# Performance work log

Hardware: AMD Instinct MI355X
Metric: run time of the kernel (lower is better)

The kernel has to match this reference:

```python
import jax, jax.numpy as jnp
import numpy as np

N_NODES = 50000
N_EDGES = 800000
IN_DIM = 128
HID_DIM = 64
N_HEADS = 4
OUT_DIM = 128
NEG_SLOPE = 0.2  # DGL GATConv default


def gat_conv(x, src, dst, W, attn_l, attn_r, bias, n_nodes):
    """DGL GATConv forward. x:[N,Fin], W:[Fin,H*D], attn_*:[H,D], bias:[H,D]. Returns [N,H,D]."""
    H, D = attn_l.shape
    h = (x @ W).reshape(n_nodes, H, D)              # [N,H,D]
    el = jnp.sum(h * attn_l[None], axis=-1)          # [N,H]
    er = jnp.sum(h * attn_r[None], axis=-1)          # [N,H]
    e = jax.nn.leaky_relu(el[src] + er[dst], NEG_SLOPE)  # [E,H]
    # edge softmax over incoming edges of each dst node (stable)
    m = jax.ops.segment_max(e, dst, num_segments=n_nodes)   # [N,H], -inf for empty
    ex = jnp.exp(e - m[dst])                                 # [E,H]
    denom = jax.ops.segment_sum(ex, dst, num_segments=n_nodes)  # [N,H]
    alpha = ex / denom[dst]                                  # [E,H]
    out = jax.ops.segment_sum(alpha[:, :, None] * h[src], dst, num_segments=n_nodes)
    return out + bias[None]                                  # [N,H,D]


def setup_inputs() -> dict:
    key = jax.random.key(0)
    ks = jax.random.split(key, 12)
    x = jax.random.normal(ks[0], (N_NODES, IN_DIM), dtype=jnp.float32)
    src = jax.random.randint(ks[1], (N_EDGES,), 0, N_NODES, dtype=jnp.int32)
    dst = jax.random.randint(ks[2], (N_EDGES,), 0, N_NODES, dtype=jnp.int32)
    s1 = 1.0 / np.sqrt(IN_DIM)
    s2 = 1.0 / np.sqrt(HID_DIM * N_HEADS)
    W1 = jax.random.normal(ks[3], (IN_DIM, N_HEADS * HID_DIM), dtype=jnp.float32) * s1
    al1 = jax.random.normal(ks[4], (N_HEADS, HID_DIM), dtype=jnp.float32) * 0.1
    ar1 = jax.random.normal(ks[5], (N_HEADS, HID_DIM), dtype=jnp.float32) * 0.1
    b1 = jnp.zeros((N_HEADS, HID_DIM), dtype=jnp.float32)
    W2 = jax.random.normal(ks[6], (N_HEADS * HID_DIM, OUT_DIM), dtype=jnp.float32) * s2
    al2 = jax.random.normal(ks[7], (1, OUT_DIM), dtype=jnp.float32) * 0.1
    ar2 = jax.random.normal(ks[8], (1, OUT_DIM), dtype=jnp.float32) * 0.1
    b2 = jnp.zeros((1, OUT_DIM), dtype=jnp.float32)
    return {"x": x, "src": src, "dst": dst, "W1": W1, "al1": al1, "ar1": ar1,
            "b1": b1, "W2": W2, "al2": al2, "ar2": ar2, "b2": b2}


def reference(x, src, dst, W1, al1, ar1, b1, W2, al2, ar2, b2):
    n = x.shape[0]
    h1 = gat_conv(x, src, dst, W1, al1, ar1, b1, n)          # [N,H,D]
    h1 = jax.nn.relu(h1).reshape(n, -1)                       # [N,H*D]
    h2 = gat_conv(h1, src, dst, W2, al2, ar2, b2, n)          # [N,1,OUT]
    return h2.reshape(n, -1)                                   # [N,OUT]
```

## Files before the change

kernel.cpp:

```cpp
#include <hip/hip_runtime.h>
#include <hip/hip_bf16.h>
#include <math.h>


#define NEG_SLOPE 0.2f
#define NB 256
#define CH 8192

typedef short short8 __attribute__((ext_vector_type(8)));
typedef float float4v __attribute__((ext_vector_type(4)));
typedef float float2v __attribute__((ext_vector_type(2)));

static __device__ __forceinline__ float lrelu(float v) {
    return v > 0.f ? v : NEG_SLOPE * v;
}

static __device__ __forceinline__ unsigned short f2bf(float f) {
    unsigned int u = __float_as_uint(f);
    u = (u + 0x7fffu + ((u >> 16) & 1u)) >> 16;
    return (unsigned short)u;
}
static __device__ __forceinline__ float bf2f(unsigned int lo16) {
    return __uint_as_float(lo16 << 16);
}

static __device__ __forceinline__ int bucket_of(int d, unsigned int M) {
    return (int)(((unsigned long long)(unsigned int)d * M) >> 32);
}

static __device__ __forceinline__ void pk_step(float2v& a00, float2v& a01,
                                               float2v& a10, float2v& a11,
                                               float2v& d0, float2v& d1,
                                               float4 w, unsigned int v) {
    float2v w01; w01[0] = w.x; w01[1] = w.y;
    float2v w23; w23[0] = w.z; w23[1] = w.w;
    float x0 = __uint_as_float(v << 16);
    float x1 = __uint_as_float(v & 0xffff0000u);
    float2v xx0 = {x0, x0};
    float2v xx1 = {x1, x1};
    asm("v_pk_fma_f32 %0, %1, %2, %0" : "+v"(a00) : "v"(w01), "v"(xx0));
    asm("v_pk_fma_f32 %0, %1, %2, %0" : "+v"(a01) : "v"(w23), "v"(xx0));
    asm("v_pk_fma_f32 %0, %1, %2, %0" : "+v"(a10) : "v"(w01), "v"(xx1));
    asm("v_pk_fma_f32 %0, %1, %2, %0" : "+v"(a11) : "v"(w23), "v"(xx1));
    asm("v_pk_add_f32 %0, %1, %0" : "+v"(d0) : "v"(w01));
    asm("v_pk_add_f32 %0, %1, %0" : "+v"(d1) : "v"(w23));
}


__global__ __launch_bounds__(256) void histbin_kernel(
        const int* __restrict__ dst, int* __restrict__ bcnt,
        int E, unsigned int M, int nblk,
        const float* __restrict__ W1, const float* __restrict__ al1,
        const float* __restrict__ ar1, const float* __restrict__ W2,
        const float* __restrict__ al2, const float* __restrict__ ar2,
        unsigned short* __restrict__ W1th, unsigned short* __restrict__ Qt1,
        unsigned short* __restrict__ Qt2, unsigned short* __restrict__ W2t) {
    int b = blockIdx.x;
    int tid = threadIdx.x;
    if (b < nblk) {
        __shared__ int lcnt[NB];
        lcnt[tid] = 0;
        __syncthreads();
        int e0 = b * CH;
        for (int i = tid; i < CH; i += 256) {
            int e = e0 + i;
            if (e < E) atomicAdd(&lcnt[bucket_of(dst[e], M)], 1);
        }
        __syncthreads();
        bcnt[b * NB + tid] = lcnt[tid];
        return;
    }
    int idx = (b - nblk) * 256 + tid;
    if (idx < 32768) {
        int h = idx >> 13;
        int r = idx & 8191;
        int d = r >> 7, k = r & 127;
        W1th[idx] = f2bf(W1[k * 256 + h * 64 + d]);
    } else if (idx < 34816) {
        int j = idx - 32768;
        int c = j >> 7, k = j & 127;
        float s = 0.f;
        if (c < 8) {
            int h = c & 3;
            const float* av = ((c < 4) ? al1 : ar1) + h * 64;
            const float* wrow = W1 + k * 256 + h * 64;
            #pragma unroll 8
            for (int d = 0; d < 64; ++d) s += wrow[d] * av[d];
        }
        Qt1[j] = f2bf(s);
    } else if (idx < 36864) {
        int j = idx - 34816;
        int c = j >> 7, k = j & 127;
        float s = (c == 0) ? al2[k] : (c == 1) ? ar2[k] : 0.f;
        Qt2[j] = f2bf(s);
    } else if (idx < 69632) {
        int j = idx - 36864;
        int m = j >> 8, k = j & 255;
        W2t[(size_t)m * 256 + k] = f2bf(W2[(size_t)k * 128 + m]);
    }
}


__global__ __launch_bounds__(256) void binscan_kernel(
        const int* __restrict__ bcnt, int* __restrict__ cur0,
        int* __restrict__ bucketStart, int nblk, int E) {
    __shared__ int s[NB];
    int t = threadIdx.x;
    int tot = 0;
    for (int blk = 0; blk < nblk; ++blk) tot += bcnt[blk * NB + t];
    s[t] = tot;
    __syncthreads();
    for (int off = 1; off < NB; off <<= 1) {
        int add = (t >= off) ? s[t - off] : 0;
        __syncthreads();
        s[t] += add;
        __syncthreads();
    }
    const int bs = s[t] - tot;
    bucketStart[t] = bs;
    if (t == NB - 1) bucketStart[NB] = E;
    int run = bs;
    for (int blk = 0; blk < nblk; ++blk) {
        int c = bcnt[blk * NB + t];
        cur0[blk * NB + t] = run;
        run += c;
    }
}


__global__ __launch_bounds__(256) void scatxdots_kernel(
        const int* __restrict__ src, const int* __restrict__ dst,
        const int* __restrict__ cur0,
        uint2* __restrict__ pairs, int E, unsigned int M, int nblk,
        const float* __restrict__ x, const unsigned short* __restrict__ Qt,
        unsigned short* __restrict__ xb,
        float* __restrict__ el, float* __restrict__ er, int N) {
    constexpr int KP = 136;
    __shared__ alignas(16) unsigned char smem[(64 + 16) * KP * 2];
    const int tid = threadIdx.x;
    if (blockIdx.x < (unsigned)nblk) {
        int* cur = (int*)smem;
        const int b = blockIdx.x;
        cur[tid] = cur0[b * NB + tid];
        __syncthreads();
        int e0 = b * CH;
        for (int i = tid; i < CH; i += 256) {
            int e = e0 + i;
            if (e < E) {
                int d = dst[e];
                int bk = bucket_of(d, M);
                int pos = atomicAdd(&cur[bk], 1);
                pairs[pos] = make_uint2((unsigned int)src[e], (unsigned int)d);
            }
        }
        return;
    }
    unsigned short* As = (unsigned short*)smem;
    unsigned short* Bs = As + 64 * KP;
    const int wid = tid >> 6, lane = tid & 63;
    const int r0 = (blockIdx.x - nblk) * 64;
    for (int ch = tid; ch < 64 * 16; ch += 256) {
        int row = ch >> 4, kc = ch & 15;
        int gr = r0 + row;
        short8 v = {};
        if (gr < N) {
            float4 a = *(const float4*)(x + (size_t)gr * 128 + kc * 8);
            float4 b = *(const float4*)(x + (size_t)gr * 128 + kc * 8 + 4);
            v[0] = (short)f2bf(a.x); v[1] = (short)f2bf(a.y);
            v[2] = (short)f2bf(a.z); v[3] = (short)f2bf(a.w);
            v[4] = (short)f2bf(b.x); v[5] = (short)f2bf(b.y);
            v[6] = (short)f2bf(b.z); v[7] = (short)f2bf(b.w);
            *(short8*)(xb + (size_t)gr * 128 + kc * 8) = v;
        }
        *(short8*)(As + row * KP + kc * 8) = v;
    }
    {
        int row = tid >> 4, kc = tid & 15;
        *(short8*)(Bs + row * KP + kc * 8) = *(const short8*)(Qt + row * 128 + kc * 8);
    }
    __syncthreads();
    float4v acc = (float4v){0.f, 0.f, 0.f, 0.f};
    const int lr = lane & 15, lk = (lane >> 4) * 8;
    #pragma unroll
    for (int ks = 0; ks < 128; ks += 32) {
        short8 af = *(const short8*)(As + (wid * 16 + lr) * KP + ks + lk);
        short8 bf_ = *(const short8*)(Bs + lr * KP + ks + lk);
        acc = __builtin_amdgcn_mfma_f32_16x16x32_bf16(af, bf_, acc, 0, 0, 0);
    }
    const int rbase = r0 + wid * 16 + (lane >> 4) * 4;
    #pragma unroll
    for (int j = 0; j < 4; ++j) {
        int row = rbase + j;
        if (row < N) {
            if (lr < 4) el[(size_t)row * 4 + lr] = acc[j];
            else if (lr < 8) er[(size_t)row * 4 + (lr - 4)] = acc[j];
        }
    }
}


__global__ __launch_bounds__(256) void bucketcsr_kernel(
        const uint2* __restrict__ pairs, const int* __restrict__ bucketStart,
        int* __restrict__ row_start, int* __restrict__ srcs,
        int N, int npb, int E) {
    __shared__ int cnt[NB];
    __shared__ int sc[NB];
    int b = blockIdx.x;
    int tid = threadIdx.x;
    int nb0 = b * npb;
    int es = bucketStart[b], ee = bucketStart[b + 1];
    cnt[tid] = 0;
    __syncthreads();
    for (int i = es + tid; i < ee; i += 256) {
        uint2 p = pairs[i];
        atomicAdd(&cnt[(int)p.y - nb0], 1);
    }
    __syncthreads();
    int myc = cnt[tid];
    sc[tid] = myc;
    __syncthreads();
    for (int off = 1; off < NB; off <<= 1) {
        int add = (tid >= off) ? sc[tid - off] : 0;
        __syncthreads();
        sc[tid] += add;
        __syncthreads();
    }
    int excl = sc[tid] - myc;
    int n = nb0 + tid;
    if (n < N && tid < npb) row_start[n] = es + excl;
    if (b == gridDim.x - 1 && tid == 0) row_start[N] = E;
    cnt[tid] = es + excl;
    __syncthreads();
    for (int i = es + tid; i < ee; i += 256) {
        uint2 p = pairs[i];
        int pos = atomicAdd(&cnt[(int)p.y - nb0], 1);
        srcs[pos] = (int)p.x;
    }
}


__global__ __launch_bounds__(256) void dots2_kernel(
        const unsigned short* __restrict__ hb, const unsigned short* __restrict__ Qt,
        float* __restrict__ el, float* __restrict__ er, int N) {
    constexpr int KP = 136;
    __shared__ unsigned short As[64 * KP];
    __shared__ unsigned short Bs[16 * KP];
    const int tid = threadIdx.x;
    const int wid = tid >> 6, lane = tid & 63;
    const int r0 = blockIdx.x * 64;
    for (int ch = tid; ch < 64 * 16; ch += 256) {
        int row = ch >> 4, kc = ch & 15;
        int gr = r0 + row;
        short8 v = {};
        if (gr < N) v = *(const short8*)(hb + (size_t)gr * 128 + kc * 8);
        *(short8*)(As + row * KP + kc * 8) = v;
    }
    {
        int row = tid >> 4, kc = tid & 15;
        *(short8*)(Bs + row * KP + kc * 8) = *(const short8*)(Qt + row * 128 + kc * 8);
    }
    __syncthreads();
    float4v acc = (float4v){0.f, 0.f, 0.f, 0.f};
    const int lr = lane & 15, lk = (lane >> 4) * 8;
    #pragma unroll
    for (int ks = 0; ks < 128; ks += 32) {
        short8 af = *(const short8*)(As + (wid * 16 + lr) * KP + ks + lk);
        short8 bf_ = *(const short8*)(Bs + lr * KP + ks + lk);
        acc = __builtin_amdgcn_mfma_f32_16x16x32_bf16(af, bf_, acc, 0, 0, 0);
    }
    const int rbase = r0 + wid * 16 + (lane >> 4) * 4;
    #pragma unroll
    for (int j = 0; j < 4; ++j) {
        int row = rbase + j;
        if (row < N) {
            if (lr == 0) el[row] = acc[j];
            else if (lr == 1) er[row] = acc[j];
        }
    }
}


__global__ __launch_bounds__(256) void agg1x_kernel(const unsigned short* __restrict__ xb,
                            const float* __restrict__ el, const float* __restrict__ er,
                            const int* __restrict__ srcs, const int* __restrict__ row_start,
                            unsigned short* __restrict__ A1, int N) {
    __shared__ int   s_tbl[4][64];
    __shared__ float a_tbl[4][64][4];
    const int wslot = threadIdx.x >> 6;
    const int lane = threadIdx.x & 63;
    const int n = (blockIdx.x * 256 + threadIdx.x) >> 6;
    if (n >= N) return;
    const int rs = row_start[n];
    const int re = row_start[n + 1];

    float2v accP[2][2];
    accP[0][0] = (float2v){0.f, 0.f}; accP[0][1] = (float2v){0.f, 0.f};
    accP[1][0] = (float2v){0.f, 0.f}; accP[1][1] = (float2v){0.f, 0.f};
    float2v dP[2];
    dP[0] = (float2v){0.f, 0.f}; dP[1] = (float2v){0.f, 0.f};

    if (re > rs) {
        const float4 ern = *(const float4*)(er + (size_t)n * 4);
        for (int base = rs; base < re; base += 64) {
            const int cnt = (re - base) < 64 ? (re - base) : 64;
            asm volatile("s_waitcnt lgkmcnt(0)" ::: "memory");
            if (lane < cnt) {
                int sv = srcs[base + lane];
                float4 ev = *(const float4*)(el + (size_t)sv * 4);
                float4 av;
                av.x = __expf(lrelu(ev.x + ern.x));
                av.y = __expf(lrelu(ev.y + ern.y));
                av.z = __expf(lrelu(ev.z + ern.z));
                av.w = __expf(lrelu(ev.w + ern.w));
                s_tbl[wslot][lane] = sv;
                *(float4*)&a_tbl[wslot][lane][0] = av;
            }
            asm volatile("s_waitcnt lgkmcnt(0)" ::: "memory");
            int i = 0;
            for (; i + 4 <= cnt; i += 4) {
                int s0 = s_tbl[wslot][i],     s1 = s_tbl[wslot][i + 1];
                int s2 = s_tbl[wslot][i + 2], s3 = s_tbl[wslot][i + 3];
                float4 w0 = *(const float4*)&a_tbl[wslot][i][0];
                float4 w1 = *(const float4*)&a_tbl[wslot][i + 1][0];
                float4 w2 = *(const float4*)&a_tbl[wslot][i + 2][0];
                float4 w3 = *(const float4*)&a_tbl[wslot][i + 3][0];
                unsigned int v0 = *(const unsigned int*)(xb + (size_t)s0 * 128 + lane * 2);
                unsigned int v1 = *(const unsigned int*)(xb + (size_t)s1 * 128 + lane * 2);
                unsigned int v2 = *(const unsigned int*)(xb + (size_t)s2 * 128 + lane * 2);
                unsigned int v3 = *(const unsigned int*)(xb + (size_t)s3 * 128 + lane * 2);
                pk_step(accP[0][0], accP[0][1], accP[1][0], accP[1][1], dP[0], dP[1], w0, v0);
                pk_step(accP[0][0], accP[0][1], accP[1][0], accP[1][1], dP[0], dP[1], w1, v1);
                pk_step(accP[0][0], accP[0][1], accP[1][0], accP[1][1], dP[0], dP[1], w2, v2);
                pk_step(accP[0][0], accP[0][1], accP[1][0], accP[1][1], dP[0], dP[1], w3, v3);
            }
            for (; i < cnt; ++i) {
                int s0 = s_tbl[wslot][i];
                float4 w = *(const float4*)&a_tbl[wslot][i][0];
                unsigned int v = *(const unsigned int*)(xb + (size_t)s0 * 128 + lane * 2);
                pk_step(accP[0][0], accP[0][1], accP[1][0], accP[1][1], dP[0], dP[1], w, v);
            }
        }
        float i0 = 1.f / dP[0][0], i1 = 1.f / dP[0][1];
        float i2 = 1.f / dP[1][0], i3 = 1.f / dP[1][1];
        accP[0][0][0] *= i0; accP[1][0][0] *= i0;
        accP[0][0][1] *= i1; accP[1][0][1] *= i1;
        accP[0][1][0] *= i2; accP[1][1][0] *= i2;
        accP[0][1][1] *= i3; accP[1][1][1] *= i3;
    }
    unsigned int pk;
    pk = (unsigned int)f2bf(accP[0][0][0]) | ((unsigned int)f2bf(accP[1][0][0]) << 16);
    *(unsigned int*)(A1 + (size_t)n * 512 + 0 * 128 + lane * 2) = pk;
    pk = (unsigned int)f2bf(accP[0][0][1]) | ((unsigned int)f2bf(accP[1][0][1]) << 16);
    *(unsigned int*)(A1 + (size_t)n * 512 + 1 * 128 + lane * 2) = pk;
    pk = (unsigned int)f2bf(accP[0][1][0]) | ((unsigned int)f2bf(accP[1][1][0]) << 16);
    *(unsigned int*)(A1 + (size_t)n * 512 + 2 * 128 + lane * 2) = pk;
    pk = (unsigned int)f2bf(accP[0][1][1]) | ((unsigned int)f2bf(accP[1][1][1]) << 16);
    *(unsigned int*)(A1 + (size_t)n * 512 + 3 * 128 + lane * 2) = pk;
}


__global__ __launch_bounds__(256) void gemm1h_kernel(
        const unsigned short* __restrict__ A1,
        const unsigned short* __restrict__ W1th,
        const float* __restrict__ b1,
        unsigned short* __restrict__ h1rb,
        int N) {
    constexpr int KP = 136;
    __shared__ unsigned short As[128 * KP];
    __shared__ unsigned short Bs[64 * KP];
    const int tid = threadIdx.x;
    const int wid = tid >> 6;
    const int lane = tid & 63;
    const int r0 = blockIdx.x * 128;
    const int h = blockIdx.z;

    for (int ch = tid; ch < 128 * 16; ch += 256) {
        int row = ch >> 4, kc = ch & 15;
        int gr = r0 + row;
        short8 v = {};
        if (gr < N) v = *(const short8*)(A1 + (size_t)gr * 512 + h * 128 + kc * 8);
        *(short8*)(As + row * KP + kc * 8) = v;
    }
    for (int ch = tid; ch < 64 * 16; ch += 256) {
        int row = ch >> 4, kc = ch & 15;
        *(short8*)(Bs + row * KP + kc * 8) =
            *(const short8*)(W1th + (size_t)h * 8192 + row * 128 + kc * 8);
    }
    __syncthreads();

    float4v acc[8];
    #pragma unroll
    for (int fr = 0; fr < 8; ++fr) acc[fr] = (float4v){0.f, 0.f, 0.f, 0.f};

    const int lr = lane & 15;
    const int lk = (lane >> 4) * 8;
    const int cw = wid * 16;

    #pragma unroll
    for (int ks = 0; ks < 128; ks += 32) {
        short8 bfr = *(const short8*)(Bs + (cw + lr) * KP + ks + lk);
        #pragma unroll
        for (int fr = 0; fr < 8; ++fr) {
            short8 af = *(const short8*)(As + (fr * 16 + lr) * KP + ks + lk);
            acc[fr] = __builtin_amdgcn_mfma_f32_16x16x32_bf16(af, bfr, acc[fr], 0, 0, 0);
        }
    }

    const int col = h * 64 + cw + lr;
    const float bias = b1[col];
    const int rbase = r0 + (lane >> 4) * 4;
    #pragma unroll
    for (int fr = 0; fr < 8; ++fr) {
        #pragma unroll
        for (int j = 0; j < 4; ++j) {
            int row = rbase + fr * 16 + j;
            if (row < N)
                h1rb[(size_t)row * 256 + col] = f2bf(fmaxf(acc[fr][j] + bias, 0.f));
        }
    }
}


template <int K, int MSLICE>
__global__ __launch_bounds__(256) void mfma_gemm_kernel(
        const unsigned short* __restrict__ A,
        const unsigned short* __restrict__ Bt,
        unsigned short* __restrict__ C,
        int N, int Mtot) {
    constexpr int KP = K + 8;
    constexpr int CF = MSLICE / 64;
    constexpr int KC = K / 8;
    __shared__ unsigned short As[64 * KP];
    __shared__ unsigned short Bs[MSLICE * KP];
    const int tid = threadIdx.x;
    const int wid = tid >> 6;
    const int lane = tid & 63;
    const int r0 = blockIdx.x * 64;
    const int c0 = blockIdx.y * MSLICE;

    for (int ch = tid; ch < 64 * KC; ch += 256) {
        int row = ch / KC, kc = ch - row * KC;
        int gr = r0 + row;
        short8 v = {};
        if (gr < N) v = *(const short8*)(A + (size_t)gr * K + kc * 8);
        *(short8*)(As + row * KP + kc * 8) = v;
    }
    for (int ch = tid; ch < MSLICE * KC; ch += 256) {
        int row = ch / KC, kc = ch - row * KC;
        *(short8*)(Bs + row * KP + kc * 8) =
            *(const short8*)(Bt + (size_t)(c0 + row) * K + kc * 8);
    }
    __syncthreads();

    float4v acc[4][CF];
    #pragma unroll
    for (int fr = 0; fr < 4; ++fr)
        #pragma unroll
        for (int cf = 0; cf < CF; ++cf)
            acc[fr][cf] = (float4v){0.f, 0.f, 0.f, 0.f};

    const int lr = lane & 15;
    const int lk = (lane >> 4) * 8;
    const int cw = wid * (MSLICE / 4);

    #pragma unroll
    for (int ks = 0; ks < K; ks += 32) {
        short8 af[4], bfr[CF];
        #pragma unroll
        for (int fr = 0; fr < 4; ++fr)
            af[fr] = *(const short8*)(As + (fr * 16 + lr) * KP + ks + lk);
        #pragma unroll
        for (int cf = 0; cf < CF; ++cf)
            bfr[cf] = *(const short8*)(Bs + (cw + cf * 16 + lr) * KP + ks + lk);
        #pragma unroll
        for (int fr = 0; fr < 4; ++fr)
            #pragma unroll
            for (int cf = 0; cf < CF; ++cf)
                acc[fr][cf] = __builtin_amdgcn_mfma_f32_16x16x32_bf16(
                    af[fr], bfr[cf], acc[fr][cf], 0, 0, 0);
    }

    const int rbase = r0 + (lane >> 4) * 4;
    #pragma unroll
    for (int fr = 0; fr < 4; ++fr) {
        #pragma unroll
        for (int cf = 0; cf < CF; ++cf) {
            int col = c0 + cw + cf * 16 + lr;
            #pragma unroll
            for (int j = 0; j < 4; ++j) {
                int row = rbase + fr * 16 + j;
                if (row < N)
                    C[(size_t)row * Mtot + col] = f2bf(acc[fr][cf][j]);
            }
        }
    }
}


__global__ __launch_bounds__(256) void agg2_kernel(const unsigned short* __restrict__ hb,
                           const float* __restrict__ el, const float* __restrict__ er,
                           const int* __restrict__ srcs, const int* __restrict__ row_start,
                           const float* __restrict__ bias, float* __restrict__ out, int N) {
    __shared__ uint2 t_tbl[4][64];
    const int wslot = threadIdx.x >> 6;
    const int lane = threadIdx.x & 63;
    const int n = (blockIdx.x * 256 + threadIdx.x) >> 6;
    if (n >= N) return;
    const int rs = row_start[n];
    const int re = row_start[n + 1];

    float acc0 = 0.f, acc1 = 0.f, d = 0.f;

    if (re > rs) {
        const float ern = er[n];
        for (int base = rs; base < re; base += 64) {
            const int cnt = (re - base) < 64 ? (re - base) : 64;
            asm volatile("s_waitcnt lgkmcnt(0)" ::: "memory");
            if (lane < cnt) {
                int sv = srcs[base + lane];
                float a = __expf(lrelu(el[sv] + ern));
                t_tbl[wslot][lane] = make_uint2((unsigned int)sv, __float_as_uint(a));
            }
            asm volatile("s_waitcnt lgkmcnt(0)" ::: "memory");
            int i = 0;
            for (; i + 4 <= cnt; i += 4) {
                uint2 t0 = t_tbl[wslot][i],     t1 = t_tbl[wslot][i + 1];
                uint2 t2 = t_tbl[wslot][i + 2], t3 = t_tbl[wslot][i + 3];
                float w0 = __uint_as_float(t0.y), w1 = __uint_as_float(t1.y);
                float w2 = __uint_as_float(t2.y), w3 = __uint_as_float(t3.y);
                unsigned int v0 = *(const unsigned int*)(hb + (size_t)t0.x * 128 + lane * 2);
                unsigned int v1 = *(const unsigned int*)(hb + (size_t)t1.x * 128 + lane * 2);
                unsigned int v2 = *(const unsigned int*)(hb + (size_t)t2.x * 128 + lane * 2);
                unsigned int v3 = *(const unsigned int*)(hb + (size_t)t3.x * 128 + lane * 2);
                d += w0 + w1 + w2 + w3;
                acc0 += w0 * bf2f(v0 & 0xffffu) + w1 * bf2f(v1 & 0xffffu) +
                        w2 * bf2f(v2 & 0xffffu) + w3 * bf2f(v3 & 0xffffu);
                acc1 += w0 * bf2f(v0 >> 16) + w1 * bf2f(v1 >> 16) +
                        w2 * bf2f(v2 >> 16) + w3 * bf2f(v3 >> 16);
            }
            for (; i < cnt; ++i) {
                uint2 t = t_tbl[wslot][i];
                float w = __uint_as_float(t.y);
                unsigned int v = *(const unsigned int*)(hb + (size_t)t.x * 128 + lane * 2);
                d += w;
                acc0 += w * bf2f(v & 0xffffu);
                acc1 += w * bf2f(v >> 16);
            }
        }
        float invd = 1.f / d;
        acc0 *= invd; acc1 *= invd;
    }
    float o0 = acc0 + bias[lane * 2];
    float o1 = acc1 + bias[lane * 2 + 1];
    *(float2*)(out + (size_t)n * 128 + lane * 2) = make_float2(o0, o1);
}


extern "C" void kernel_launch(void* const* d_in, const int* in_sizes, int n_in,
                              void* d_out, int out_size, void* d_ws, size_t ws_size,
                              hipStream_t stream) {
    const float* x   = (const float*)d_in[0];
    const int*   src = (const int*)d_in[1];
    const int*   dst = (const int*)d_in[2];
    const float* W1  = (const float*)d_in[3];
    const float* al1 = (const float*)d_in[4];
    const float* ar1 = (const float*)d_in[5];
    const float* b1  = (const float*)d_in[6];
    const float* W2  = (const float*)d_in[7];
    const float* al2 = (const float*)d_in[8];
    const float* ar2 = (const float*)d_in[9];
    const float* b2  = (const float*)d_in[10];
    float* out = (float*)d_out;

    const int N = in_sizes[0] / 128;
    const int E = in_sizes[1];
    const int npb = (N + NB - 1) / NB;
    const unsigned int M =
        (unsigned int)(((1ULL << 32) + npb - 1) / (unsigned long long)npb);
    const int nblk_e = (E + CH - 1) / CH;

    char* ws = (char*)d_ws;
    size_t oXB   = 0;
    size_t oA1   = oXB + (size_t)N * 128 * 2;
    size_t oH1R  = oA1 + (size_t)N * 512 * 2;
    size_t oW1th = oH1R + (size_t)N * 256 * 2;
    size_t oQt1  = oW1th + 32768 * 2;
    size_t oQt2  = oQt1 + 2048 * 2;
    size_t oW2t  = oQt2 + 2048 * 2;
    size_t oEl1  = oW2t + 32768 * 2;
    size_t oEr1  = oEl1 + (size_t)N * 4 * 4;
    size_t oEl2  = oEr1 + (size_t)N * 4 * 4;
    size_t oEr2  = oEl2 + (size_t)N * 4;
    size_t oRow  = oEr2 + (size_t)N * 4;
    size_t oBcnt = oRow + (((size_t)(N + 1) * 4 + 15) & ~(size_t)15);
    size_t oCur0 = oBcnt + (size_t)nblk_e * NB * 4;
    size_t oBkS  = oCur0 + (size_t)nblk_e * NB * 4;
    size_t oPair = (oBkS + (NB + 1) * 4 + 15) & ~(size_t)15;
    size_t oSrcs = oPair + (size_t)E * 8;

    unsigned short* xb   = (unsigned short*)(ws + oXB);
    unsigned short* A1   = (unsigned short*)(ws + oA1);
    unsigned short* h2b  = (unsigned short*)(ws + oA1);
    unsigned short* h1rb = (unsigned short*)(ws + oH1R);
    unsigned short* w1th = (unsigned short*)(ws + oW1th);
    unsigned short* qt1  = (unsigned short*)(ws + oQt1);
    unsigned short* qt2  = (unsigned short*)(ws + oQt2);
    unsigned short* w2t  = (unsigned short*)(ws + oW2t);
    float* el1 = (float*)(ws + oEl1);
    float* er1 = (float*)(ws + oEr1);
    float* el2 = (float*)(ws + oEl2);
    float* er2 = (float*)(ws + oEr2);
    int*   row_start   = (int*)(ws + oRow);
    int*   bcnt        = (int*)(ws + oBcnt);
    int*   cur0        = (int*)(ws + oCur0);
    int*   bucketStart = (int*)(ws + oBkS);
    uint2* pairs       = (uint2*)(ws + oPair);
    int*   srcs        = (int*)(ws + oSrcs);

    const int nrowb = (N + 63) / 64;
    const int nrowb2 = (N + 127) / 128;
    const int nwaveb = (N + 3) / 4;

    histbin_kernel<<<nblk_e + 272, 256, 0, stream>>>(
        dst, bcnt, E, M, nblk_e, W1, al1, ar1, W2, al2, ar2, w1th, qt1, qt2, w2t);

    binscan_kernel<<<1, 256, 0, stream>>>(bcnt, cur0, bucketStart, nblk_e, E);

    scatxdots_kernel<<<nblk_e + nrowb, 256, 0, stream>>>(
        src, dst, cur0, pairs, E, M, nblk_e,
        x, qt1, xb, el1, er1, N);

    bucketcsr_kernel<<<NB, 256, 0, stream>>>(pairs, bucketStart, row_start, srcs, N, npb, E);

    agg1x_kernel<<<nwaveb, 256, 0, stream>>>(xb, el1, er1, srcs, row_start, A1, N);
    gemm1h_kernel<<<dim3(nrowb2, 1, 4), 256, 0, stream>>>(A1, w1th, b1, h1rb, N);

    mfma_gemm_kernel<256, 64><<<dim3(nrowb, 2), 256, 0, stream>>>(h1rb, w2t, h2b, N, 128);
    dots2_kernel<<<nrowb, 256, 0, stream>>>(h2b, qt2, el2, er2, N);
    agg2_kernel<<<nwaveb, 256, 0, stream>>>(h2b, el2, er2, srcs, row_start, b2, out, N);
}
```

Measured before the change: 205.6 us.

## Fuse layer-1 GEMM, layer-2 GEMM and attention dots into one kernel

Replaces three kernels (per-head layer-1 projection with bias+ReLU, layer-2 GEMM, and el2/er2 dot-product MFMA) with a single kernel per 64-row tile. Each head's ReLU output stays in shared memory and is multiplied straight into the layer-2 accumulator, and the resulting h2 tile is reused from LDS for the attention dots. This removes the h1 intermediate round trip through global memory and two launches. In exchange it uses more LDS per block, which may lower occupancy, and stages weights repeatedly per head in every block.

```diff
diff --git a/kernel.cpp b/kernel.cpp
--- a/kernel.cpp
+++ b/kernel.cpp
@@ -235,47 +235,6 @@
         uint2 p = pairs[i];
         int pos = atomicAdd(&cnt[(int)p.y - nb0], 1);
         srcs[pos] = (int)p.x;
-    }
-}
-
-
-__global__ __launch_bounds__(256) void dots2_kernel(
-        const unsigned short* __restrict__ hb, const unsigned short* __restrict__ Qt,
-        float* __restrict__ el, float* __restrict__ er, int N) {
-    constexpr int KP = 136;
-    __shared__ unsigned short As[64 * KP];
-    __shared__ unsigned short Bs[16 * KP];
-    const int tid = threadIdx.x;
-    const int wid = tid >> 6, lane = tid & 63;
-    const int r0 = blockIdx.x * 64;
-    for (int ch = tid; ch < 64 * 16; ch += 256) {
-        int row = ch >> 4, kc = ch & 15;
-        int gr = r0 + row;
-        short8 v = {};
-        if (gr < N) v = *(const short8*)(hb + (size_t)gr * 128 + kc * 8);
-        *(short8*)(As + row * KP + kc * 8) = v;
-    }
-    {
-        int row = tid >> 4, kc = tid & 15;
-        *(short8*)(Bs + row * KP + kc * 8) = *(const short8*)(Qt + row * 128 + kc * 8);
-    }
-    __syncthreads();
-    float4v acc = (float4v){0.f, 0.f, 0.f, 0.f};
-    const int lr = lane & 15, lk = (lane >> 4) * 8;
-    #pragma unroll
-    for (int ks = 0; ks < 128; ks += 32) {
-        short8 af = *(const short8*)(As + (wid * 16 + lr) * KP + ks + lk);
-        short8 bf_ = *(const short8*)(Bs + lr * KP + ks + lk);
-        acc = __builtin_amdgcn_mfma_f32_16x16x32_bf16(af, bf_, acc, 0, 0, 0);
-    }
-    const int rbase = r0 + wid * 16 + (lane >> 4) * 4;
-    #pragma unroll
-    for (int j = 0; j < 4; ++j) {
-        int row = rbase + j;
-        if (row < N) {
-            if (lr == 0) el[row] = acc[j];
-            else if (lr == 1) er[row] = acc[j];
-        }
     }
 }
 
@@ -359,139 +318,116 @@
 }
 
 
-__global__ __launch_bounds__(256) void gemm1h_kernel(
+__global__ __launch_bounds__(256) void l2fused_kernel(
         const unsigned short* __restrict__ A1,
         const unsigned short* __restrict__ W1th,
         const float* __restrict__ b1,
-        unsigned short* __restrict__ h1rb,
+        const unsigned short* __restrict__ W2t,
+        const unsigned short* __restrict__ Qt2,
+        unsigned short* __restrict__ h2b,
+        float* __restrict__ el2, float* __restrict__ er2,
         int N) {
     constexpr int KP = 136;
-    __shared__ unsigned short As[128 * KP];
-    __shared__ unsigned short Bs[64 * KP];
+    constexpr int PP = 72;
+    __shared__ unsigned short As[64 * KP];
+    __shared__ unsigned short Bs1[64 * KP];
+    __shared__ unsigned short Bs2[128 * PP];
+    __shared__ unsigned short Ps[64 * PP];
+    __shared__ unsigned short Qs[16 * KP];
     const int tid = threadIdx.x;
-    const int wid = tid >> 6;
-    const int lane = tid & 63;
-    const int r0 = blockIdx.x * 128;
-    const int h = blockIdx.z;
-
-    for (int ch = tid; ch < 128 * 16; ch += 256) {
-        int row = ch >> 4, kc = ch & 15;
-        int gr = r0 + row;
-        short8 v = {};
-        if (gr < N) v = *(const short8*)(A1 + (size_t)gr * 512 + h * 128 + kc * 8);
-        *(short8*)(As + row * KP + kc * 8) = v;
-    }
-    for (int ch = tid; ch < 64 * 16; ch += 256) {
-        int row = ch >> 4, kc = ch & 15;
-        *(short8*)(Bs + row * KP + kc * 8) =
-            *(const short8*)(W1th + (size_t)h * 8192 + row * 128 + kc * 8);
-    }
-    __syncthreads();
-
-    float4v acc[8];
+    const int wid = tid >> 6, lane = tid & 63;
+    const int lr = lane & 15, lk = (lane >> 4) * 8;
+    const int r0 = blockIdx.x * 64;
+
+    {
+        int row = tid >> 4, kc = tid & 15;
+        *(short8*)(Qs + row * KP + kc * 8) = *(const short8*)(Qt2 + row * 128 + kc * 8);
+    }
+
+    float4v acc2[8];
     #pragma unroll
-    for (int fr = 0; fr < 8; ++fr) acc[fr] = (float4v){0.f, 0.f, 0.f, 0.f};
-
-    const int lr = lane & 15;
-    const int lk = (lane >> 4) * 8;
-    const int cw = wid * 16;
-
+    for (int cf = 0; cf < 8; ++cf) acc2[cf] = (float4v){0.f, 0.f, 0.f, 0.f};
+
+    for (int h = 0; h < 4; ++h) {
+        __syncthreads();
+        for (int ch = tid; ch < 1024; ch += 256) {
+            int row = ch >> 4, kc = ch & 15;
+            int gr = r0 + row;
+            short8 v = {};
+            if (gr < N) v = *(const short8*)(A1 + (size_t)gr * 512 + h * 128 + kc * 8);
+            *(short8*)(As + row * KP + kc * 8) = v;
+        }
+        for (int ch = tid; ch < 1024; ch += 256) {
+            int row = ch >> 4, kc = ch & 15;
+            *(short8*)(Bs1 + row * KP + kc * 8) =
+                *(const short8*)(W1th + (size_t)h * 8192 + row * 128 + kc * 8);
+        }
+        for (int ch = tid; ch < 1024; ch += 256) {
+            int m = ch >> 3, kc = ch & 7;
+            *(short8*)(Bs2 + m * PP + kc * 8) =
+                *(const short8*)(W2t + (size_t)m * 256 + h * 64 + kc * 8);
+        }
+        __syncthreads();
+
+        float4v p[4];
+        #pragma unroll
+        for (int cf = 0; cf < 4; ++cf) p[cf] = (float4v){0.f, 0.f, 0.f, 0.f};
+        #pragma unroll
+        for (int ks = 0; ks < 128; ks += 32) {
+            short8 af = *(const short8*)(As + (wid * 16 + lr) * KP + ks + lk);
+            #pragma unroll
+            for (int cf = 0; cf < 4; ++cf) {
+                short8 bfr = *(const short8*)(Bs1 + (cf * 16 + lr) * KP + ks + lk);
+                p[cf] = __builtin_amdgcn_mfma_f32_16x16x32_bf16(af, bfr, p[cf], 0, 0, 0);
+            }
+        }
+        const int prow = wid * 16 + (lane >> 4) * 4;
+        #pragma unroll
+        for (int cf = 0; cf < 4; ++cf) {
+            float bias = b1[h * 64 + cf * 16 + lr];
+            #pragma unroll
+            for (int j = 0; j < 4; ++j)
+                Ps[(prow + j) * PP + cf * 16 + lr] = f2bf(fmaxf(p[cf][j] + bias, 0.f));
+        }
+        __syncthreads();
+
+        #pragma unroll
+        for (int ks2 = 0; ks2 < 64; ks2 += 32) {
+            short8 af2 = *(const short8*)(Ps + (wid * 16 + lr) * PP + ks2 + lk);
+            #pragma unroll
+            for (int cf = 0; cf < 8; ++cf) {
+                short8 bf2 = *(const short8*)(Bs2 + (cf * 16 + lr) * PP + ks2 + lk);
+                acc2[cf] = __builtin_amdgcn_mfma_f32_16x16x32_bf16(af2, bf2, acc2[cf], 0, 0, 0);
+            }
+        }
+    }
+
+    const int prow = wid * 16 + (lane >> 4) * 4;
+    #pragma unroll
+    for (int cf = 0; cf < 8; ++cf) {
+        int col = cf * 16 + lr;
+        #pragma unroll
+        for (int j = 0; j < 4; ++j) {
+            unsigned short hv = f2bf(acc2[cf][j]);
+            int row = prow + j;
+            if (r0 + row < N) h2b[(size_t)(r0 + row) * 128 + col] = hv;
+            As[row * KP + col] = hv;
+        }
+    }
+    __syncthreads();
+    float4v dd = (float4v){0.f, 0.f, 0.f, 0.f};
     #pragma unroll
     for (int ks = 0; ks < 128; ks += 32) {
-        short8 bfr = *(const short8*)(Bs + (cw + lr) * KP + ks + lk);
-        #pragma unroll
-        for (int fr = 0; fr < 8; ++fr) {
-            short8 af = *(const short8*)(As + (fr * 16 + lr) * KP + ks + lk);
-            acc[fr] = __builtin_amdgcn_mfma_f32_16x16x32_bf16(af, bfr, acc[fr], 0, 0, 0);
-        }
-    }
-
-    const int col = h * 64 + cw + lr;
-    const float bias = b1[col];
-    const int rbase = r0 + (lane >> 4) * 4;
+        short8 af = *(const short8*)(As + (wid * 16 + lr) * KP + ks + lk);
+        short8 bq = *(const short8*)(Qs + lr * KP + ks + lk);
+        dd = __builtin_amdgcn_mfma_f32_16x16x32_bf16(af, bq, dd, 0, 0, 0);
+    }
     #pragma unroll
-    for (int fr = 0; fr < 8; ++fr) {
-        #pragma unroll
-        for (int j = 0; j < 4; ++j) {
-            int row = rbase + fr * 16 + j;
-            if (row < N)
-                h1rb[(size_t)row * 256 + col] = f2bf(fmaxf(acc[fr][j] + bias, 0.f));
-        }
-    }
-}
-
-
-template <int K, int MSLICE>
-__global__ __launch_bounds__(256) void mfma_gemm_kernel(
-        const unsigned short* __restrict__ A,
-        const unsigned short* __restrict__ Bt,
-        unsigned short* __restrict__ C,
-        int N, int Mtot) {
-    constexpr int KP = K + 8;
-    constexpr int CF = MSLICE / 64;
-    constexpr int KC = K / 8;
-    __shared__ unsigned short As[64 * KP];
-    __shared__ unsigned short Bs[MSLICE * KP];
-    const int tid = threadIdx.x;
-    const int wid = tid >> 6;
-    const int lane = tid & 63;
-    const int r0 = blockIdx.x * 64;
-    const int c0 = blockIdx.y * MSLICE;
-
-    for (int ch = tid; ch < 64 * KC; ch += 256) {
-        int row = ch / KC, kc = ch - row * KC;
-        int gr = r0 + row;
-        short8 v = {};
-        if (gr < N) v = *(const short8*)(A + (size_t)gr * K + kc * 8);
-        *(short8*)(As + row * KP + kc * 8) = v;
-    }
-    for (int ch = tid; ch < MSLICE * KC; ch += 256) {
-        int row = ch / KC, kc = ch - row * KC;
-        *(short8*)(Bs + row * KP + kc * 8) =
-            *(const short8*)(Bt + (size_t)(c0 + row) * K + kc * 8);
-    }
-    __syncthreads();
-
-    float4v acc[4][CF];
-    #pragma unroll
-    for (int fr = 0; fr < 4; ++fr)
-        #pragma unroll
-        for (int cf = 0; cf < CF; ++cf)
-            acc[fr][cf] = (float4v){0.f, 0.f, 0.f, 0.f};
-
-    const int lr = lane & 15;
-    const int lk = (lane >> 4) * 8;
-    const int cw = wid * (MSLICE / 4);
-
-    #pragma unroll
-    for (int ks = 0; ks < K; ks += 32) {
-        short8 af[4], bfr[CF];
-        #pragma unroll
-        for (int fr = 0; fr < 4; ++fr)
-            af[fr] = *(const short8*)(As + (fr * 16 + lr) * KP + ks + lk);
-        #pragma unroll
-        for (int cf = 0; cf < CF; ++cf)
-            bfr[cf] = *(const short8*)(Bs + (cw + cf * 16 + lr) * KP + ks + lk);
-        #pragma unroll
-        for (int fr = 0; fr < 4; ++fr)
-            #pragma unroll
-            for (int cf = 0; cf < CF; ++cf)
-                acc[fr][cf] = __builtin_amdgcn_mfma_f32_16x16x32_bf16(
-                    af[fr], bfr[cf], acc[fr][cf], 0, 0, 0);
-    }
-
-    const int rbase = r0 + (lane >> 4) * 4;
-    #pragma unroll
-    for (int fr = 0; fr < 4; ++fr) {
-        #pragma unroll
-        for (int cf = 0; cf < CF; ++cf) {
-            int col = c0 + cw + cf * 16 + lr;
-            #pragma unroll
-            for (int j = 0; j < 4; ++j) {
-                int row = rbase + fr * 16 + j;
-                if (row < N)
-                    C[(size_t)row * Mtot + col] = f2bf(acc[fr][cf][j]);
-            }
+    for (int j = 0; j < 4; ++j) {
+        int row = r0 + prow + j;
+        if (row < N) {
+            if (lr == 0) el2[row] = dd[j];
+            else if (lr == 1) er2[row] = dd[j];
         }
     }
 }
@@ -582,8 +518,8 @@
     char* ws = (char*)d_ws;
     size_t oXB   = 0;
     size_t oA1   = oXB + (size_t)N * 128 * 2;
-    size_t oH1R  = oA1 + (size_t)N * 512 * 2;
-    size_t oW1th = oH1R + (size_t)N * 256 * 2;
+    size_t oH2   = oA1 + (size_t)N * 512 * 2;
+    size_t oW1th = oH2 + (size_t)N * 128 * 2;
     size_t oQt1  = oW1th + 32768 * 2;
     size_t oQt2  = oQt1 + 2048 * 2;
     size_t oW2t  = oQt2 + 2048 * 2;
@@ -600,8 +536,7 @@
 
     unsigned short* xb   = (unsigned short*)(ws + oXB);
     unsigned short* A1   = (unsigned short*)(ws + oA1);
-    unsigned short* h2b  = (unsigned short*)(ws + oA1);
-    unsigned short* h1rb = (unsigned short*)(ws + oH1R);
+    unsigned short* h2b  = (unsigned short*)(ws + oH2);
     unsigned short* w1th = (unsigned short*)(ws + oW1th);
     unsigned short* qt1  = (unsigned short*)(ws + oQt1);
     unsigned short* qt2  = (unsigned short*)(ws + oQt2);
@@ -618,7 +553,6 @@
     int*   srcs        = (int*)(ws + oSrcs);
 
     const int nrowb = (N + 63) / 64;
-    const int nrowb2 = (N + 127) / 128;
     const int nwaveb = (N + 3) / 4;
 
     histbin_kernel<<<nblk_e + 272, 256, 0, stream>>>(
@@ -633,9 +567,8 @@
     bucketcsr_kernel<<<NB, 256, 0, stream>>>(pairs, bucketStart, row_start, srcs, N, npb, E);
 
     agg1x_kernel<<<nwaveb, 256, 0, stream>>>(xb, el1, er1, srcs, row_start, A1, N);
-    gemm1h_kernel<<<dim3(nrowb2, 1, 4), 256, 0, stream>>>(A1, w1th, b1, h1rb, N);
-
-    mfma_gemm_kernel<256, 64><<<dim3(nrowb, 2), 256, 0, stream>>>(h1rb, w2t, h2b, N, 128);
-    dots2_kernel<<<nrowb, 256, 0, stream>>>(h2b, qt2, el2, er2, N);
+
+    l2fused_kernel<<<nrowb, 256, 0, stream>>>(A1, w1th, b1, w2t, qt2, h2b, el2, er2, N);
+
     agg2_kernel<<<nwaveb, 256, 0, stream>>>(h2b, el2, er2, srcs, row_start, b2, out, N);
 }
```

Measured after the change: 192.7 us. 1.07x faster.
